# Performance work log

Hardware: AMD Instinct MI355X
Metric: run time of the kernel (lower is better)

## Reference

```python
import jax, jax.numpy as jnp
import numpy as np

NU, NS, NT = 200000, 100000, 100000
N = NS + NU + NT          # node order: [source items | users | target items]
D = 32                    # embedding_size
K = 3                     # graph_layer_K
DK = D * (K + 1)          # 128, concat of all propagation layers
META = 64                 # meta_dim
B = 2048                  # batch
L = 50                    # padded history length
NNZ = 2000000             # nnz of normalized adjacency


def setup_inputs() -> dict:
    key = jax.random.key(0)
    ks = jax.random.split(key, 32)
    f = lambda i, shape, s=0.05: jax.random.normal(ks[i], shape, jnp.float32) * s
    z = lambda shape: jnp.zeros(shape, jnp.float32)
    return dict(
        u=jax.random.randint(ks[0], (B,), 0, NU, jnp.int32),
        si=jax.random.randint(ks[1], (B,), 0, NS, jnp.int32),
        ti=jax.random.randint(ks[2], (B,), 0, NT, jnp.int32),
        src_seq=jax.random.randint(ks[3], (NU, L), 0, NS, jnp.int32),
        tgt_seq=jax.random.randint(ks[4], (NU, L), 0, NT, jnp.int32),
        adj_rows=jax.random.randint(ks[5], (NNZ,), 0, N, jnp.int32),
        adj_cols=jax.random.randint(ks[6], (NNZ,), 0, N, jnp.int32),
        adj_vals=jax.random.uniform(ks[7], (NNZ,), jnp.float32) * 0.1,
        user_emb=f(8, (NU, D), 0.1),
        item_s_emb=f(9, (NS, D), 0.1),
        item_t_emb=f(10, (NT, D), 0.1),
        attn_s_w1=f(11, (D, D)), attn_s_b1=z((D,)), attn_s_w2=f(12, (D, 1)),
        attn_t_w1=f(13, (D, D)), attn_t_b1=z((D,)), attn_t_w2=f(14, (D, 1)),
        dec_ss_w1=f(15, (D, META)), dec_ss_b1=z((META,)),
        dec_ss_w2=f(16, (META, DK * DK), 0.02), dec_ss_b2=z((DK * DK,)),
        dec_tt_w1=f(17, (D, META)), dec_tt_b1=z((META,)),
        dec_tt_w2=f(18, (META, DK * DK), 0.02), dec_tt_b2=z((DK * DK,)),
        mlp_s_w1=f(19, (2 * DK, 128)), mlp_s_b1=z((128,)),
        mlp_s_w2=f(20, (128, 64)), mlp_s_b2=z((64,)),
        dense_s_w=f(21, (64, 1)), dense_s_b=z((1,)),
        mlp_t_w1=f(22, (2 * DK, 128)), mlp_t_b1=z((128,)),
        mlp_t_w2=f(23, (128, 64)), mlp_t_b2=z((64,)),
        dense_t_w=f(24, (64, 1)), dense_t_b=z((1,)),
    )


def _attn_pool(seq_ids, item_emb, w1, b1, w2):
    # masked attention pooling over padded history; pad id is 0
    e = item_emb[seq_ids]                          # [B,L,D]
    h = jax.nn.relu(e @ w1 + b1)                   # attention_layer_K = 1
    logits = h @ w2                                # [B,L,1], no bias on final layer
    mask = (seq_ids == 0)[..., None].astype(e.dtype)
    att = jax.nn.softmax(logits - mask * 1e8, axis=1)
    return jnp.sum(att * e, axis=1)                # [B,D]


def _meta_decode(his, w1, b1, w2, b2, u_e):
    # meta-generated per-sample DKxDK transform applied to the user embedding
    W = (jax.nn.relu(his @ w1 + b1) @ w2 + b2).reshape(-1, DK, DK)
    return jnp.einsum('bd,bde->be', u_e, W)


def _ncf(x, w1, b1, w2, b2, dw, db):
    h = jax.nn.relu(x @ w1 + b1)
    h = jax.nn.relu(h @ w2 + b2)
    return jax.nn.sigmoid(h @ dw + db)[:, 0]


def reference(u, si, ti, src_seq, tgt_seq, adj_rows, adj_cols, adj_vals,
              user_emb, item_s_emb, item_t_emb,
              attn_s_w1, attn_s_b1, attn_s_w2, attn_t_w1, attn_t_b1, attn_t_w2,
              dec_ss_w1, dec_ss_b1, dec_ss_w2, dec_ss_b2,
              dec_tt_w1, dec_tt_b1, dec_tt_w2, dec_tt_b2,
              mlp_s_w1, mlp_s_b1, mlp_s_w2, mlp_s_b2, dense_s_w, dense_s_b,
              mlp_t_w1, mlp_t_b1, mlp_t_w2, mlp_t_b2, dense_t_w, dense_t_b):
    his_s = _attn_pool(src_seq[u], item_s_emb, attn_s_w1, attn_s_b1, attn_s_w2)
    his_t = _attn_pool(tgt_seq[u], item_t_emb, attn_t_w1, attn_t_b1, attn_t_w2)

    # 'raw' graph encoder: K hops of sparse A @ E over [item_s | user | item_t]
    emb = jnp.concatenate([item_s_emb, user_emb, item_t_emb], axis=0)  # [N,D]
    all_emb = [emb]
    for _ in range(K):
        emb = jax.ops.segment_sum(adj_vals[:, None] * emb[adj_cols], adj_rows,
                                  num_segments=N)
        all_emb.append(emb)
    all_e = jnp.concatenate(all_emb, axis=1)       # [N, DK]

    si_e = all_e[si]                               # source items: rows [0, NS)
    u_e = all_e[NS + u]                            # users: rows [NS, NS+NU)
    ti_e = all_e[NS + NU + ti]                     # target items

    u_ss = _meta_decode(his_s, dec_ss_w1, dec_ss_b1, dec_ss_w2, dec_ss_b2, u_e)
    u_tt = _meta_decode(his_t, dec_tt_w1, dec_tt_b1, dec_tt_w2, dec_tt_b2, u_e)

    pred_s = _ncf(jnp.concatenate([u_ss, si_e], -1),
                  mlp_s_w1, mlp_s_b1, mlp_s_w2, mlp_s_b2, dense_s_w, dense_s_b)
    pred_t = _ncf(jnp.concatenate([u_tt, ti_e], -1),
                  mlp_t_w1, mlp_t_b1, mlp_t_w2, mlp_t_b2, dense_t_w, dense_t_b)
    return jnp.stack([pred_s, pred_t])             # [2, B]
```

## Files before the change

kernel.cpp:

```cpp
#include <hip/hip_runtime.h>
#include <hip/hip_bf16.h>

#define NU_ 200000
#define NS_ 100000
#define NT_ 100000
#define NN_ (NS_ + NU_ + NT_)
#define D_ 32
#define DK_ 128
#define META_ 64
#define B_ 2048
#define L_ 50
#define NNZ_ 2000000
#define GK_ 8192

#define RPB_ 391
#define NB_ 1024
#define STAGE_CAP_ 4096
#define CAPA_ 1280
#define CAPB_ 512

#define SB_EMB_   6250
#define IN4_SLOT3_ 100096
#define IN4_MARKS_ 50048
#define IN4_E3C_   49152
#define IN4_TOT_  (IN4_SLOT3_ + IN4_MARKS_ + IN4_E3C_)
#define SB_INIT_  ((IN4_TOT_ + 2048 + 255) / 256)
#define SB_TOT_   (SB_EMB_ + SB_INIT_)

#define PB_GATHER_ 192
#define PB_HRELU_  (PB_GATHER_ + 1024)
#define PB_TOT_    (PB_HRELU_ + 1024)

#define NCF_TILE_ 16

typedef __attribute__((ext_vector_type(8))) short bf16x8;
typedef __attribute__((ext_vector_type(4))) float f32x4;

__device__ inline unsigned bfpack(float a, float b) {
    unsigned r;
    asm("v_cvt_pk_bf16_f32 %0, %1, %2" : "=v"(r) : "v"(a), "v"(b));
    return r;
}
__device__ inline float bf2f(short s) {
    return __uint_as_float(((unsigned)(unsigned short)s) << 16);
}

__global__ __launch_bounds__(256) void setup_kernel(
    const float* __restrict__ item_s, const float* __restrict__ user_e,
    const float* __restrict__ item_t, unsigned short* __restrict__ tab,
    int* __restrict__ slot3, int* __restrict__ marks ,
    float* __restrict__ E3c, int* __restrict__ bcurA, int* __restrict__ bcurB)
{
    int bid = blockIdx.x, t = threadIdx.x;
    if (bid < SB_EMB_) {
        int tid = bid * 256 + t;
        int row = tid >> 2, seg = tid & 3;
        const float* src;
        if (row < NS_)            src = item_s + (size_t)row * 32;
        else if (row < NS_ + NU_) src = user_e + (size_t)(row - NS_) * 32;
        else                      src = item_t + (size_t)(row - NS_ - NU_) * 32;
        const float4* sp = (const float4*)(src + seg * 8);
        float4 a = sp[0], b = sp[1];
        uint4 r;
        r.x = bfpack(a.x, a.y); r.y = bfpack(a.z, a.w);
        r.z = bfpack(b.x, b.y); r.w = bfpack(b.z, b.w);
        *(uint4*)(tab + (size_t)row * 32 + seg * 8) = r;
    } else {
        int idx = (bid - SB_EMB_) * 256 + t;
        if (idx < IN4_SLOT3_) {
            ((int4*)slot3)[idx] = make_int4(-1, -1, -1, -1);
        } else if (idx < IN4_SLOT3_ + IN4_MARKS_) {
            ((int4*)marks)[idx - IN4_SLOT3_] = make_int4(0, 0, 0, 0);
        } else if (idx < IN4_TOT_) {
            ((int4*)E3c)[idx - IN4_SLOT3_ - IN4_MARKS_] = make_int4(0, 0, 0, 0);
        } else {
            int c = idx - IN4_TOT_;
            if (c < NB_)            bcurA[c] = c * CAPA_;
            else if (c < 2 * NB_)   bcurB[c - NB_] = (c - NB_) * CAPB_;
        }
    }
}

__global__ __launch_bounds__(256) void mark_seeds(
    const int* __restrict__ u, const int* __restrict__ si, const int* __restrict__ ti,
    int* __restrict__ slot3, unsigned char* __restrict__ mark1,
    unsigned char* __restrict__ mark2)
{
    int n = blockIdx.x * 256 + threadIdx.x;
    if (n >= 3 * B_) return;
    int which = n >> 11, b = n & (B_ - 1);
    int row = (which == 0) ? si[b] : (which == 1) ? NS_ + u[b] : NS_ + NU_ + ti[b];
    slot3[row] = n;
    mark1[row] = 1;
    mark2[row] = 1;
}

__global__ __launch_bounds__(256) void mark_pass(
    const int* __restrict__ rows, const int* __restrict__ cols,
    const int* __restrict__ slot3, const unsigned char* __restrict__ msrc,
    unsigned char* __restrict__ mdst, int use_slot)
{
    int j = blockIdx.x * 256 + threadIdx.x;
    if (j >= NNZ_) return;
    int r = rows[j];
    bool cond = use_slot ? (slot3[r] >= 0) : (msrc[r] != 0);
    if (cond) mdst[cols[j]] = 1;
}

__global__ __launch_bounds__(512) void partition_edges(
    const int* __restrict__ rows, const int* __restrict__ cols,
    const float* __restrict__ vals,
    const unsigned char* __restrict__ mark1, const unsigned char* __restrict__ mark2,
    int* __restrict__ bcurA, int* __restrict__ bcurB,
    int2* __restrict__ partA, int2* __restrict__ partB)
{
    __shared__ int hist[NB_], sstart[NB_], sbase[NB_], scur[NB_];
    __shared__ int2 stage[STAGE_CAP_];
    __shared__ unsigned short stageb[STAGE_CAP_];
    __shared__ int stotal;

    int t = threadIdx.x;
    for (int i = t; i < NB_; i += 512) hist[i] = 0;
    __syncthreads();

    int base = blockIdx.x * 8192;
    int mybkt[16]; int2 mye[16]; unsigned myB = 0;
    #pragma unroll
    for (int i = 0; i < 16; i++) {
        int j = base + i * 512 + t;
        mybkt[i] = -1;
        if (j < NNZ_) {
            int r = rows[j];
            if (mark1[r]) {
                int bb = r / RPB_;
                int lr = r - bb * RPB_;
                mye[i] = make_int2((lr << 19) | cols[j], __float_as_int(vals[j]));
                mybkt[i] = bb;
                if (mark2[r]) myB |= (1u << i);
                atomicAdd(&hist[bb], 1);
            }
        }
    }
    __syncthreads();
    for (int i = t; i < NB_; i += 512) sstart[i] = hist[i];
    __syncthreads();
    for (int off = 1; off < NB_; off <<= 1) {
        int x0 = (t >= off) ? sstart[t - off] : 0;
        int x1 = (t + 512 >= off) ? sstart[t + 512 - off] : 0;
        __syncthreads();
        sstart[t] += x0; sstart[t + 512] += x1;
        __syncthreads();
    }
    if (t == 0) stotal = sstart[NB_ - 1];
    __syncthreads();
    int tot = stotal;
    for (int i = t; i < NB_; i += 512) {
        int cnt = hist[i];
        sstart[i] -= cnt;
        sbase[i] = cnt ? atomicAdd(&bcurA[i], cnt) : 0;
        scur[i] = 0;
    }
    __syncthreads();

    if (tot <= STAGE_CAP_) {
        #pragma unroll
        for (int i = 0; i < 16; i++) {
            int bb = mybkt[i];
            if (bb >= 0) {
                int p = atomicAdd(&scur[bb], 1);
                int s = sstart[bb] + p;
                stage[s] = mye[i];
                stageb[s] = (unsigned short)bb;
            }
        }
        __syncthreads();
        for (int i = t; i < tot; i += 512) {
            int bb = stageb[i];
            int pos = sbase[bb] + (i - sstart[bb]);
            if (pos < (bb + 1) * CAPA_) partA[pos] = stage[i];
        }
    } else {
        #pragma unroll
        for (int i = 0; i < 16; i++) {
            int bb = mybkt[i];
            if (bb >= 0) {
                int p = atomicAdd(&scur[bb], 1);
                int pos = sbase[bb] + p;
                if (pos < (bb + 1) * CAPA_) partA[pos] = mye[i];
            }
        }
    }
    __syncthreads();
    for (int i = t; i < NB_; i += 512) hist[i] = 0;
    __syncthreads();
    #pragma unroll
    for (int i = 0; i < 16; i++)
        if (myB & (1u << i)) atomicAdd(&hist[mybkt[i]], 1);
    __syncthreads();
    for (int i = t; i < NB_; i += 512) {
        sbase[i] = hist[i] ? atomicAdd(&bcurB[i], hist[i]) : 0;
        scur[i] = 0;
    }
    __syncthreads();
    #pragma unroll
    for (int i = 0; i < 16; i++) {
        if (myB & (1u << i)) {
            int bb = mybkt[i];
            int p = atomicAdd(&scur[bb], 1);
            int pos = sbase[bb] + p;
            if (pos < (bb + 1) * CAPB_) partB[pos] = mye[i];
        }
    }
}

__global__ __launch_bounds__(512) void hop_csr(
    const int* __restrict__ bcur, const int2* __restrict__ part, int cap,
    const unsigned short* __restrict__ tab,
    const unsigned char* __restrict__ markw,
    const int* __restrict__ fgate,
    float* __restrict__ yf, unsigned short* __restrict__ ybf)
{
    __shared__ int2 sorted[CAPA_];
    __shared__ int cnt[RPB_];
    __shared__ int scanb[512];

    int t = threadIdx.x;
    int bkt = blockIdx.x;
    int e0 = bkt * cap;
    int n = bcur[bkt] - e0;
    if (n > cap) n = cap;

    for (int i = t; i < RPB_; i += 512) cnt[i] = 0;
    __syncthreads();
    for (int i = t; i < n; i += 512) {
        int lr = (part[e0 + i].x >> 19) & 0x3FF;
        atomicAdd(&cnt[lr], 1);
    }
    __syncthreads();
    scanb[t] = (t < RPB_) ? cnt[t] : 0;
    __syncthreads();
    for (int off = 1; off < 512; off <<= 1) {
        int x = (t >= off) ? scanb[t - off] : 0;
        __syncthreads();
        scanb[t] += x;
        __syncthreads();
    }
    if (t < RPB_) cnt[t] = scanb[t] - cnt[t];
    __syncthreads();
    for (int i = t; i < n; i += 512) {
        int2 e = part[e0 + i];
        int lr = (e.x >> 19) & 0x3FF;
        int p2 = atomicAdd(&cnt[lr], 1);
        sorted[p2] = e;
    }
    __syncthreads();
    int chunk = t & 3;
    int row0 = bkt * RPB_;
    for (int r = t >> 2; r < RPB_; r += 128) {
        int grow = row0 + r;
        if (grow >= NN_ || !markw[grow]) continue;
        int eb = (r == 0) ? 0 : scanb[r - 1];
        int ee = scanb[r];
        float racc[8] = {0.f, 0.f, 0.f, 0.f, 0.f, 0.f, 0.f, 0.f};
        for (int e = eb; e < ee; e++) {
            int2 ed = sorted[e];
            int col = ed.x & 0x7FFFF;
            float vv = __int_as_float(ed.y);
            bf16x8 x = *(const bf16x8*)(tab + (size_t)col * 32 + chunk * 8);
            #pragma unroll
            for (int k = 0; k < 8; k++) racc[k] += vv * bf2f(x[k]);
        }
        float4 o0 = {racc[0], racc[1], racc[2], racc[3]};
        float4 o1 = {racc[4], racc[5], racc[6], racc[7]};
        if (!fgate || fgate[grow] >= 0) {
            float4* yp = (float4*)(yf + (size_t)grow * 32 + chunk * 8);
            yp[0] = o0; yp[1] = o1;
        }
        if (ybf) {
            uint4 pk;
            pk.x = bfpack(o0.x, o0.y); pk.y = bfpack(o0.z, o0.w);
            pk.z = bfpack(o1.x, o1.y); pk.w = bfpack(o1.z, o1.w);
            *(uint4*)(ybf + (size_t)grow * 32 + chunk * 8) = pk;
        }
    }
}

__global__ __launch_bounds__(256) void hop3_part(
    const int* __restrict__ bcurB, const int2* __restrict__ partB,
    const int* __restrict__ slot3,
    const float* __restrict__ E2, float* __restrict__ E3c)
{
    int t = threadIdx.x;
    int bkt = blockIdx.x;
    int e0 = bkt * CAPB_;
    int e1 = bcurB[bkt];
    int emax = e0 + CAPB_;
    if (e1 > emax) e1 = emax;
    int c = t & 7;
    for (int i = e0 + (t >> 3); i < e1; i += 32) {
        int2 e = partB[i];
        int lr = (e.x >> 19) & 0x3FF;
        int s = slot3[bkt * RPB_ + lr];
        if (s < 0) continue;
        int col = e.x & 0x7FFFF;
        float v = __int_as_float(e.y);
        float4 xv = ((const float4*)E2)[(size_t)col * 8 + c];
        float* p = E3c + (size_t)s * 32 + c * 4;
        unsafeAtomicAdd(p + 0, v * xv.x);
        unsafeAtomicAdd(p + 1, v * xv.y);
        unsafeAtomicAdd(p + 2, v * xv.z);
        unsafeAtomicAdd(p + 3, v * xv.w);
    }
}

__global__ __launch_bounds__(64) void attn_pool(
    const int* __restrict__ u,
    const int* __restrict__ seq_s, const int* __restrict__ seq_t,
    const float* __restrict__ emb_s, const float* __restrict__ emb_t,
    const float* __restrict__ w1_s, const float* __restrict__ b1_s,
    const float* __restrict__ w2_s,
    const float* __restrict__ w1_t, const float* __restrict__ b1_t,
    const float* __restrict__ w2_t,
    float* __restrict__ out_s, float* __restrict__ out_t)
{
    int b = blockIdx.x, dom = blockIdx.y;
    const int* seq = dom ? seq_t : seq_s;
    const float* emb = dom ? emb_t : emb_s;
    const float* w1 = dom ? w1_t : w1_s;
    const float* b1 = dom ? b1_t : b1_s;
    const float* w2 = dom ? w2_t : w2_s;
    float* out = dom ? out_t : out_s;

    int l = threadIdx.x;
    __shared__ float w1s[32 * 32];
    __shared__ float b1s[32];
    __shared__ float w2s[32];
    __shared__ float es[L_ * 32];
    __shared__ float att[64];

    for (int i = l; i < 1024; i += 64) w1s[i] = w1[i];
    if (l < 32) { b1s[l] = b1[l]; w2s[l] = w2[l]; }
    __syncthreads();

    int uid = u[b];
    float logit = -1e30f;
    if (l < L_) {
        int id = seq[uid * L_ + l];
        const float4* ep = (const float4*)(emb + (size_t)id * 32);
        float e[32];
        #pragma unroll
        for (int q = 0; q < 8; q++) {
            float4 v = ep[q];
            e[4*q+0] = v.x; e[4*q+1] = v.y; e[4*q+2] = v.z; e[4*q+3] = v.w;
        }
        float acc = 0.f;
        #pragma unroll
        for (int i = 0; i < 32; i++) {
            float h = b1s[i];
            #pragma unroll
            for (int jj = 0; jj < 32; jj++) h += e[jj] * w1s[jj * 32 + i];
            h = fmaxf(h, 0.f);
            acc += h * w2s[i];
        }
        logit = acc - (id == 0 ? 1e8f : 0.f);
        #pragma unroll
        for (int jj = 0; jj < 32; jj++) es[l * 32 + jj] = e[jj];
    }
    float m = logit;
    for (int off = 32; off > 0; off >>= 1) m = fmaxf(m, __shfl_down(m, off, 64));
    m = __shfl(m, 0, 64);
    float ex = (l < L_) ? expf(logit - m) : 0.f;
    float s = ex;
    for (int off = 32; off > 0; off >>= 1) s += __shfl_down(s, off, 64);
    s = __shfl(s, 0, 64);
    att[l] = ex / s;
    __syncthreads();

    if (l < 32) {
        float o = 0.f;
        for (int q = 0; q < L_; q++) o += att[q] * es[q * 32 + l];
        out[b * 32 + l] = o;
    }
}

__global__ __launch_bounds__(256) void prep_kernel(
    const float* __restrict__ E1, const float* __restrict__ E2,
    const float* __restrict__ E3c, const int* __restrict__ slot3,
    const int* __restrict__ u, const int* __restrict__ si, const int* __restrict__ ti,
    const float* __restrict__ user_emb, const float* __restrict__ item_s,
    const float* __restrict__ item_t,
    float* __restrict__ u_e, float* __restrict__ si_e, float* __restrict__ ti_e,
    const float* __restrict__ his_s, const float* __restrict__ his_t,
    const float* __restrict__ dw1_s, const float* __restrict__ db1_s,
    const float* __restrict__ dw1_t, const float* __restrict__ db1_t,
    float* __restrict__ h_s, float* __restrict__ h_t,
    const float* __restrict__ w2_s, const float* __restrict__ w2_t,
    unsigned short* __restrict__ o_s, unsigned short* __restrict__ o_t)
{
    int bid = blockIdx.x, t = threadIdx.x;
    if (bid < PB_GATHER_) {
        int tid = bid * 256 + t;
        if (tid >= 3 * B_ * 8) return;
        int n = tid >> 3, c = tid & 7;
        int which = n >> 11, b = n & (B_ - 1);
        int row;
        const float4* base0;
        float* outp;
        if (which == 0)      { int id = si[b]; row = id;             base0 = (const float4*)item_s + (size_t)id * 8; outp = si_e; }
        else if (which == 1) { int id = u[b];  row = NS_ + id;       base0 = (const float4*)user_emb + (size_t)id * 8; outp = u_e; }
        else                 { int id = ti[b]; row = NS_ + NU_ + id; base0 = (const float4*)item_t + (size_t)id * 8; outp = ti_e; }
        float4 k0 = base0[c];
        float4 k1 = ((const float4*)E1)[(size_t)row * 8 + c];
        float4 k2 = ((const float4*)E2)[(size_t)row * 8 + c];
        float4 k3 = ((const float4*)E3c)[(size_t)slot3[row] * 8 + c];
        float4* orow = (float4*)(outp + (size_t)b * 128);
        orow[0 * 8 + c] = k0;
        orow[1 * 8 + c] = k1;
        orow[2 * 8 + c] = k2;
        orow[3 * 8 + c] = k3;
    } else if (bid < PB_HRELU_) {
        int b2 = bid - PB_GATHER_;
        int dom = b2 >> 9, sub = b2 & 511;
        const float* his = dom ? his_t : his_s;
        const float* w1  = dom ? dw1_t : dw1_s;
        const float* b1  = dom ? db1_t : db1_s;
        float* h         = dom ? h_t   : h_s;
        int b = sub * 4 + (t >> 6);
        int m = t & 63;
        float acc = b1[m];
        #pragma unroll
        for (int j = 0; j < 32; j++) acc += his[b * 32 + j] * w1[j * 64 + m];
        h[b * 64 + m] = fmaxf(acc, 0.f);
    } else {
        int b3 = bid - PB_HRELU_;
        int dom = b3 >> 9, sub = b3 & 511;
        const float* w2 = dom ? w2_t : w2_s;
        unsigned short* o = dom ? o_t : o_s;
        int tid = sub * 256 + t;
        int nn = tid & 127, k8 = tid >> 7;
        float v[8];
        #pragma unroll
        for (int i = 0; i < 8; i++) v[i] = w2[(size_t)(k8 * 8 + i) * 128 + nn];
        uint4 r;
        r.x = bfpack(v[0], v[1]); r.y = bfpack(v[2], v[3]);
        r.z = bfpack(v[4], v[5]); r.w = bfpack(v[6], v[7]);
        *(uint4*)(o + (size_t)nn * GK_ + k8 * 8) = r;
    }
}

__global__ __launch_bounds__(256) void meta_gemm(
    const float* __restrict__ h_s, const float* __restrict__ h_t,
    const float* __restrict__ ue,
    const unsigned short* __restrict__ w2t_s, const unsigned short* __restrict__ w2t_t,
    float* __restrict__ P)
{
    __shared__ unsigned short As[64 * 72];
    __shared__ unsigned short Bs[128 * 72];

    int mt = blockIdx.x & 31, dom = blockIdx.x >> 5;
    int ks = blockIdx.y;
    const float* h = dom ? h_t : h_s;
    const unsigned short* w2t = dom ? w2t_t : w2t_s;

    int t = threadIdx.x;
    int ar = t >> 2, aseg = t & 3;
    int bn = t >> 1, bhalf = t & 1;
    int w = t >> 6, lane = t & 63;
    int quad = lane >> 4, l16 = lane & 15;
    int wm = (w & 1) * 32, wn = (w >> 1) * 64;

    f32x4 acc[8];
    #pragma unroll
    for (int i = 0; i < 8; i++) { acc[i][0]=0.f; acc[i][1]=0.f; acc[i][2]=0.f; acc[i][3]=0.f; }

    for (int ch = 0; ch < 16; ch++) {
        int kb = ks * 1024 + ch * 64;
        __syncthreads();
        {
            int gm = mt * 64 + ar;
            int m_idx = kb >> 7;
            int d0 = (kb & 127) + aseg * 16;
            float hv = h[gm * 64 + m_idx];
            const float4* up = (const float4*)(ue + (size_t)gm * 128 + d0);
            float4 x0 = up[0], x1 = up[1], x2 = up[2], x3 = up[3];
            uint4 A0, A1;
            A0.x = bfpack(hv*x0.x, hv*x0.y); A0.y = bfpack(hv*x0.z, hv*x0.w);
            A0.z = bfpack(hv*x1.x, hv*x1.y); A0.w = bfpack(hv*x1.z, hv*x1.w);
            A1.x = bfpack(hv*x2.x, hv*x2.y); A1.y = bfpack(hv*x2.z, hv*x2.w);
            A1.z = bfpack(hv*x3.x, hv*x3.y); A1.w = bfpack(hv*x3.z, hv*x3.w);
            uint4* sa = (uint4*)(As + ar * 72 + aseg * 16);
            sa[0] = A0; sa[1] = A1;
        }
        {
            const uint4* gb = (const uint4*)(w2t + (size_t)bn * GK_ + kb + bhalf * 32);
            uint4* sb = (uint4*)(Bs + bn * 72 + bhalf * 32);
            sb[0] = gb[0]; sb[1] = gb[1]; sb[2] = gb[2]; sb[3] = gb[3];
        }
        __syncthreads();
        #pragma unroll
        for (int kk = 0; kk < 2; kk++) {
            int ko = kk * 32 + quad * 8;
            bf16x8 a0 = *(const bf16x8*)(As + (wm + l16) * 72 + ko);
            bf16x8 a1 = *(const bf16x8*)(As + (wm + 16 + l16) * 72 + ko);
            #pragma unroll
            for (int nt = 0; nt < 4; nt++) {
                bf16x8 bfr = *(const bf16x8*)(Bs + (wn + nt * 16 + l16) * 72 + ko);
                acc[nt]     = __builtin_amdgcn_mfma_f32_16x16x32_bf16(a0, bfr, acc[nt],     0, 0, 0);
                acc[4 + nt] = __builtin_amdgcn_mfma_f32_16x16x32_bf16(a1, bfr, acc[4 + nt], 0, 0, 0);
            }
        }
    }
    float* op = P + ((size_t)dom * 8 + ks) * B_ * 128;
    #pragma unroll
    for (int ma = 0; ma < 2; ma++)
        #pragma unroll
        for (int nt = 0; nt < 4; nt++) {
            int row = mt * 64 + wm + ma * 16 + quad * 4;
            int col = wn + nt * 16 + l16;
            f32x4 v = acc[ma * 4 + nt];
            op[(size_t)(row + 0) * 128 + col] = v[0];
            op[(size_t)(row + 1) * 128 + col] = v[1];
            op[(size_t)(row + 2) * 128 + col] = v[2];
            op[(size_t)(row + 3) * 128 + col] = v[3];
        }
}

__global__ __launch_bounds__(512) void ncf_kernel(
    const float* __restrict__ P, const float* __restrict__ u_e,
    const float* __restrict__ b2_s, const float* __restrict__ b2_t,
    const float* __restrict__ si_e, const float* __restrict__ ti_e,
    const float* __restrict__ w1_s, const float* __restrict__ b1_s,
    const float* __restrict__ w2_s, const float* __restrict__ bb2_s,
    const float* __restrict__ dw_s, const float* __restrict__ db_s,
    const float* __restrict__ w1_t, const float* __restrict__ b1_t,
    const float* __restrict__ w2_t, const float* __restrict__ bb2_t,
    const float* __restrict__ dw_t, const float* __restrict__ db_t,
    float* __restrict__ out)
{
    int tile = blockIdx.x, dom = blockIdx.y, t = threadIdx.x;
    int b0 = tile * NCF_TILE_;
    const float* Pd     = P + (size_t)dom * 8 * B_ * 128;
    const float* b2meta = dom ? b2_t : b2_s;
    const float* pair_e = dom ? ti_e : si_e;
    const float* w1 = dom ? w1_t : w1_s;
    const float* b1 = dom ? b1_t : b1_s;
    const float* w2 = dom ? w2_t : w2_s;
    const float* bb2 = dom ? bb2_t : bb2_s;
    const float* dw = dom ? dw_t : dw_s;
    const float* db = dom ? db_t : db_s;

    __shared__ float ues[NCF_TILE_ * 128];
    __shared__ float xs[NCF_TILE_ * 256];
    __shared__ float h1s[NCF_TILE_ * 128];
    __shared__ float h2s[NCF_TILE_ * 64];

    {
        float4 v = ((const float4*)(u_e + (size_t)b0 * 128))[t];
        ((float4*)ues)[t] = v;
        float4 pv = ((const float4*)(pair_e + (size_t)b0 * 128))[t];
        int s = t >> 5, c4 = t & 31;
        ((float4*)(xs + s * 256 + 128))[c4] = pv;
    }
    __syncthreads();

    int j = t & 127, g = t >> 7;
    {
        float acc[4];
        #pragma unroll
        for (int ss = 0; ss < 4; ss++) {
            int b = b0 + g * 4 + ss;
            float a = 0.f;
            #pragma unroll
            for (int ks = 0; ks < 8; ks++)
                a += Pd[(size_t)ks * B_ * 128 + (size_t)b * 128 + j];
            acc[ss] = a;
        }
        for (int dc = 0; dc < 32; dc++) {
            float wa = b2meta[(dc * 4 + 0) * 128 + j];
            float wb = b2meta[(dc * 4 + 1) * 128 + j];
            float wc = b2meta[(dc * 4 + 2) * 128 + j];
            float wd = b2meta[(dc * 4 + 3) * 128 + j];
            #pragma unroll
            for (int ss = 0; ss < 4; ss++) {
                float4 uv = ((const float4*)(ues + (g * 4 + ss) * 128))[dc];
                acc[ss] += uv.x * wa + uv.y * wb + uv.z * wc + uv.w * wd;
            }
        }
        #pragma unroll
        for (int ss = 0; ss < 4; ss++) xs[(g * 4 + ss) * 256 + j] = acc[ss];
    }
    __syncthreads();

    {
        float b1v = b1[j];
        float acc[4] = {b1v, b1v, b1v, b1v};
        for (int kc = 0; kc < 64; kc++) {
            float wa = w1[(kc * 4 + 0) * 128 + j];
            float wb = w1[(kc * 4 + 1) * 128 + j];
            float wc = w1[(kc * 4 + 2) * 128 + j];
            float wd = w1[(kc * 4 + 3) * 128 + j];
            #pragma unroll
            for (int ss = 0; ss < 4; ss++) {
                float4 xv = ((const float4*)(xs + (g * 4 + ss) * 256))[kc];
                acc[ss] += xv.x * wa + xv.y * wb + xv.z * wc + xv.w * wd;
            }
        }
        #pragma unroll
        for (int ss = 0; ss < 4; ss++)
            h1s[(g * 4 + ss) * 128 + j] = fmaxf(acc[ss], 0.f);
    }
    __syncthreads();

    {
        int m = t & 63, g2 = t >> 6;
        float bv = bb2[m];
        float acc[2] = {bv, bv};
        for (int kc = 0; kc < 32; kc++) {
            float wa = w2[(kc * 4 + 0) * 64 + m];
            float wb = w2[(kc * 4 + 1) * 64 + m];
            float wc = w2[(kc * 4 + 2) * 64 + m];
            float wd = w2[(kc * 4 + 3) * 64 + m];
            #pragma unroll
            for (int ss = 0; ss < 2; ss++) {
                float4 hv = ((const float4*)(h1s + (g2 * 2 + ss) * 128))[kc];
                acc[ss] += hv.x * wa + hv.y * wb + hv.z * wc + hv.w * wd;
            }
        }
        #pragma unroll
        for (int ss = 0; ss < 2; ss++)
            h2s[(g2 * 2 + ss) * 64 + m] = fmaxf(acc[ss], 0.f);
    }
    __syncthreads();

    {
        int s = t >> 5, l = t & 31;
        float sum = h2s[s * 64 + l] * dw[l] + h2s[s * 64 + 32 + l] * dw[32 + l];
        #pragma unroll
        for (int off = 16; off > 0; off >>= 1) sum += __shfl_down(sum, off, 32);
        if (l == 0) {
            float z = sum + db[0];
            out[(size_t)dom * B_ + b0 + s] = 1.f / (1.f + expf(-z));
        }
    }
}

extern "C" void kernel_launch(void* const* d_in, const int* in_sizes, int n_in,
                              void* d_out, int out_size, void* d_ws, size_t ws_size,
                              hipStream_t stream)
{
    const int*   u          = (const int*)  d_in[0];
    const int*   si         = (const int*)  d_in[1];
    const int*   ti         = (const int*)  d_in[2];
    const int*   src_seq    = (const int*)  d_in[3];
    const int*   tgt_seq    = (const int*)  d_in[4];
    const int*   adj_rows   = (const int*)  d_in[5];
    const int*   adj_cols   = (const int*)  d_in[6];
    const float* adj_vals   = (const float*)d_in[7];
    const float* user_emb   = (const float*)d_in[8];
    const float* item_s_emb = (const float*)d_in[9];
    const float* item_t_emb = (const float*)d_in[10];
    const float* attn_s_w1  = (const float*)d_in[11];
    const float* attn_s_b1  = (const float*)d_in[12];
    const float* attn_s_w2  = (const float*)d_in[13];
    const float* attn_t_w1  = (const float*)d_in[14];
    const float* attn_t_b1  = (const float*)d_in[15];
    const float* attn_t_w2  = (const float*)d_in[16];
    const float* dec_ss_w1  = (const float*)d_in[17];
    const float* dec_ss_b1  = (const float*)d_in[18];
    const float* dec_ss_w2  = (const float*)d_in[19];
    const float* dec_ss_b2  = (const float*)d_in[20];
    const float* dec_tt_w1  = (const float*)d_in[21];
    const float* dec_tt_b1  = (const float*)d_in[22];
    const float* dec_tt_w2  = (const float*)d_in[23];
    const float* dec_tt_b2  = (const float*)d_in[24];
    const float* mlp_s_w1   = (const float*)d_in[25];
    const float* mlp_s_b1   = (const float*)d_in[26];
    const float* mlp_s_w2   = (const float*)d_in[27];
    const float* mlp_s_b2   = (const float*)d_in[28];
    const float* dense_s_w  = (const float*)d_in[29];
    const float* dense_s_b  = (const float*)d_in[30];
    const float* mlp_t_w1   = (const float*)d_in[31];
    const float* mlp_t_b1   = (const float*)d_in[32];
    const float* mlp_t_w2   = (const float*)d_in[33];
    const float* mlp_t_b2   = (const float*)d_in[34];
    const float* dense_t_w  = (const float*)d_in[35];
    const float* dense_t_b  = (const float*)d_in[36];

    char* p = (char*)d_ws;
    float* E1    = (float*)p;              p += (size_t)NN_ * 32 * 4;
    float* E2    = (float*)p;              p += (size_t)NN_ * 32 * 4;
    unsigned short* Ebf  = (unsigned short*)p; p += (size_t)NN_ * 32 * 2;
    unsigned short* E1bf = (unsigned short*)p; p += (size_t)NN_ * 32 * 2;
    int2*  partA = (int2*)p;               p += (size_t)NB_ * CAPA_ * 8;
    int2*  partB = (int2*)p;               p += (size_t)NB_ * CAPB_ * 8;
    int*   slot3 = (int*)p;                p += (size_t)400384 * 4;
    int*   marks = (int*)p;
    unsigned char* mark1 = (unsigned char*)p; p += 400384;
    unsigned char* mark2 = (unsigned char*)p; p += 400384;
    float* E3c   = (float*)p;              p += (size_t)3 * B_ * 32 * 4;
    int*   bcurA = (int*)p;                p += NB_ * 4;
    int*   bcurB = (int*)p;                p += NB_ * 4;
    float* his_s = (float*)p;              p += (size_t)B_ * 32 * 4;
    float* his_t = (float*)p;              p += (size_t)B_ * 32 * 4;
    float* u_e   = (float*)p;              p += (size_t)B_ * 128 * 4;
    float* si_e  = (float*)p;              p += (size_t)B_ * 128 * 4;
    float* ti_e  = (float*)p;              p += (size_t)B_ * 128 * 4;
    float* h_s   = (float*)p;              p += (size_t)B_ * 64 * 4;
    float* h_t   = (float*)p;              p += (size_t)B_ * 64 * 4;
    float* P     = (float*)p;              p += (size_t)2 * 8 * B_ * 128 * 4;
    unsigned short* w2t_s = (unsigned short*)p; p += (size_t)128 * GK_ * 2;
    unsigned short* w2t_t = (unsigned short*)p; p += (size_t)128 * GK_ * 2;

    int nnzBlocks = (NNZ_ + 255) / 256;

    setup_kernel<<<SB_TOT_, 256, 0, stream>>>(item_s_emb, user_emb, item_t_emb,
                                              Ebf, slot3, marks, E3c, bcurA, bcurB);
    mark_seeds<<<24, 256, 0, stream>>>(u, si, ti, slot3, mark1, mark2);
    mark_pass<<<nnzBlocks, 256, 0, stream>>>(adj_rows, adj_cols, slot3, mark2, mark2, 1);
    mark_pass<<<nnzBlocks, 256, 0, stream>>>(adj_rows, adj_cols, slot3, mark2, mark1, 0);
    partition_edges<<<245, 512, 0, stream>>>(adj_rows, adj_cols, adj_vals,
                                             mark1, mark2, bcurA, bcurB, partA, partB);
    hop_csr<<<NB_, 512, 0, stream>>>(bcurA, partA, CAPA_, Ebf,  mark1, slot3, E1, E1bf);
    hop_csr<<<NB_, 512, 0, stream>>>(bcurB, partB, CAPB_, E1bf, mark2, nullptr, E2, nullptr);
    hop3_part<<<NB_, 256, 0, stream>>>(bcurB, partB, slot3, E2, E3c);
    attn_pool<<<dim3(B_, 2), 64, 0, stream>>>(u, src_seq, tgt_seq,
                                              item_s_emb, item_t_emb,
                                              attn_s_w1, attn_s_b1, attn_s_w2,
                                              attn_t_w1, attn_t_b1, attn_t_w2,
                                              his_s, his_t);
    prep_kernel<<<PB_TOT_, 256, 0, stream>>>(E1, E2, E3c, slot3, u, si, ti,
                                             user_emb, item_s_emb, item_t_emb,
                                             u_e, si_e, ti_e,
                                             his_s, his_t,
                                             dec_ss_w1, dec_ss_b1,
                                             dec_tt_w1, dec_tt_b1, h_s, h_t,
                                             dec_ss_w2, dec_tt_w2, w2t_s, w2t_t);
    meta_gemm<<<dim3(64, 8), 256, 0, stream>>>(h_s, h_t, u_e, w2t_s, w2t_t, P);
    ncf_kernel<<<dim3(B_ / NCF_TILE_, 2), 512, 0, stream>>>(P, u_e, dec_ss_b2, dec_tt_b2,
                                                si_e, ti_e,
                                                mlp_s_w1, mlp_s_b1, mlp_s_w2, mlp_s_b2,
                                                dense_s_w, dense_s_b,
                                                mlp_t_w1, mlp_t_b1, mlp_t_w2, mlp_t_b2,
                                                dense_t_w, dense_t_b,
                                                (float*)d_out);
}
```

Measured before the change: 421.1 us.

## Fold attention pooling and W2 transpose into setup kernel; register-cache edges in hop_csr

The attention-pooling kernel is merged into setup_kernel as extra blocks, each handling four batch rows with one wave apiece, and the decoder W2 bf16 transpose moves from prep_kernel into setup_kernel as well. This drops one launch and lets independent work share the first kernel's grid. hop_csr now loads each thread's up to three edges into registers once and reuses them for both the counting and scatter passes, avoiding a second global read of the partition. setup_kernel's shared memory grows, since every block allocates the attention buffers, which may lower occupancy for the large embedding-conversion part of its grid.

```diff
diff --git a/kernel.cpp b/kernel.cpp
--- a/kernel.cpp
+++ b/kernel.cpp
@@ -26,10 +26,12 @@
 #define IN4_TOT_  (IN4_SLOT3_ + IN4_MARKS_ + IN4_E3C_)
 #define SB_INIT_  ((IN4_TOT_ + 2048 + 255) / 256)
 #define SB_TOT_   (SB_EMB_ + SB_INIT_)
+#define SB_ATT0_  SB_TOT_
+#define SB_W2C0_  (SB_TOT_ + 1024)
+#define SB_GRID_  (SB_W2C0_ + 1024)
 
 #define PB_GATHER_ 192
-#define PB_HRELU_  (PB_GATHER_ + 1024)
-#define PB_TOT_    (PB_HRELU_ + 1024)
+#define PB_TOT_    (PB_GATHER_ + 1024)
 
 #define NCF_TILE_ 16
 
@@ -49,8 +51,23 @@
     const float* __restrict__ item_s, const float* __restrict__ user_e,
     const float* __restrict__ item_t, unsigned short* __restrict__ tab,
     int* __restrict__ slot3, int* __restrict__ marks ,
-    float* __restrict__ E3c, int* __restrict__ bcurA, int* __restrict__ bcurB)
-{
+    float* __restrict__ E3c, int* __restrict__ bcurA, int* __restrict__ bcurB,
+    const int* __restrict__ u,
+    const int* __restrict__ seq_s, const int* __restrict__ seq_t,
+    const float* __restrict__ aw1_s, const float* __restrict__ ab1_s,
+    const float* __restrict__ aw2_s,
+    const float* __restrict__ aw1_t, const float* __restrict__ ab1_t,
+    const float* __restrict__ aw2_t,
+    float* __restrict__ his_s, float* __restrict__ his_t,
+    const float* __restrict__ dw2_s, const float* __restrict__ dw2_t,
+    unsigned short* __restrict__ o_s, unsigned short* __restrict__ o_t)
+{
+    __shared__ float w1s[1024];
+    __shared__ float b1s[32];
+    __shared__ float w2s[32];
+    __shared__ float es[4][L_ * 32];
+    __shared__ float att[4][64];
+
     int bid = blockIdx.x, t = threadIdx.x;
     if (bid < SB_EMB_) {
         int tid = bid * 256 + t;
@@ -65,7 +82,7 @@
         r.x = bfpack(a.x, a.y); r.y = bfpack(a.z, a.w);
         r.z = bfpack(b.x, b.y); r.w = bfpack(b.z, b.w);
         *(uint4*)(tab + (size_t)row * 32 + seg * 8) = r;
-    } else {
+    } else if (bid < SB_TOT_) {
         int idx = (bid - SB_EMB_) * 256 + t;
         if (idx < IN4_SLOT3_) {
             ((int4*)slot3)[idx] = make_int4(-1, -1, -1, -1);
@@ -78,6 +95,75 @@
             if (c < NB_)            bcurA[c] = c * CAPA_;
             else if (c < 2 * NB_)   bcurB[c - NB_] = (c - NB_) * CAPB_;
         }
+    } else if (bid < SB_W2C0_) {
+        int aid = bid - SB_ATT0_;
+        int dom = aid >> 9;
+        const int* seq = dom ? seq_t : seq_s;
+        const float* emb = dom ? item_t : item_s;
+        const float* w1 = dom ? aw1_t : aw1_s;
+        const float* b1 = dom ? ab1_t : ab1_s;
+        const float* w2 = dom ? aw2_t : aw2_s;
+        float* out = dom ? his_t : his_s;
+
+        for (int i = t; i < 1024; i += 256) w1s[i] = w1[i];
+        if (t < 32) { b1s[t] = b1[t]; w2s[t] = w2[t]; }
+        __syncthreads();
+
+        int w = t >> 6, l = t & 63;
+        int b = (aid & 511) * 4 + w;
+        int uid = u[b];
+        float logit = -1e30f;
+        if (l < L_) {
+            int id = seq[uid * L_ + l];
+            const float4* ep = (const float4*)(emb + (size_t)id * 32);
+            float e[32];
+            #pragma unroll
+            for (int q = 0; q < 8; q++) {
+                float4 v = ep[q];
+                e[4*q+0] = v.x; e[4*q+1] = v.y; e[4*q+2] = v.z; e[4*q+3] = v.w;
+            }
+            float acc = 0.f;
+            #pragma unroll
+            for (int i = 0; i < 32; i++) {
+                float h = b1s[i];
+                #pragma unroll
+                for (int jj = 0; jj < 32; jj++) h += e[jj] * w1s[jj * 32 + i];
+                h = fmaxf(h, 0.f);
+                acc += h * w2s[i];
+            }
+            logit = acc - (id == 0 ? 1e8f : 0.f);
+            #pragma unroll
+            for (int jj = 0; jj < 32; jj++) es[w][l * 32 + jj] = e[jj];
+        }
+        float m = logit;
+        for (int off = 32; off > 0; off >>= 1) m = fmaxf(m, __shfl_down(m, off, 64));
+        m = __shfl(m, 0, 64);
+        float ex = (l < L_) ? expf(logit - m) : 0.f;
+        float s = ex;
+        for (int off = 32; off > 0; off >>= 1) s += __shfl_down(s, off, 64);
+        s = __shfl(s, 0, 64);
+        att[w][l] = ex / s;
+        __syncthreads();
+
+        if (l < 32) {
+            float o = 0.f;
+            for (int q = 0; q < L_; q++) o += att[w][q] * es[w][q * 32 + l];
+            out[b * 32 + l] = o;
+        }
+    } else {
+        int b3 = bid - SB_W2C0_;
+        int dom = b3 >> 9, sub = b3 & 511;
+        const float* w2 = dom ? dw2_t : dw2_s;
+        unsigned short* o = dom ? o_t : o_s;
+        int tid = sub * 256 + t;
+        int nn = tid & 127, k8 = tid >> 7;
+        float v[8];
+        #pragma unroll
+        for (int i = 0; i < 8; i++) v[i] = w2[(size_t)(k8 * 8 + i) * 128 + nn];
+        uint4 r;
+        r.x = bfpack(v[0], v[1]); r.y = bfpack(v[2], v[3]);
+        r.z = bfpack(v[4], v[5]); r.w = bfpack(v[6], v[7]);
+        *(uint4*)(o + (size_t)nn * GK_ + k8 * 8) = r;
     }
 }
 
@@ -230,12 +316,21 @@
     int n = bcur[bkt] - e0;
     if (n > cap) n = cap;
 
+    int2 mye[3]; int myl[3];
+    #pragma unroll
+    for (int i = 0; i < 3; i++) {
+        int j = i * 512 + t;
+        myl[i] = -1;
+        if (j < n) {
+            mye[i] = part[e0 + j];
+            myl[i] = (mye[i].x >> 19) & 0x3FF;
+        }
+    }
     for (int i = t; i < RPB_; i += 512) cnt[i] = 0;
     __syncthreads();
-    for (int i = t; i < n; i += 512) {
-        int lr = (part[e0 + i].x >> 19) & 0x3FF;
-        atomicAdd(&cnt[lr], 1);
-    }
+    #pragma unroll
+    for (int i = 0; i < 3; i++)
+        if (myl[i] >= 0) atomicAdd(&cnt[myl[i]], 1);
     __syncthreads();
     scanb[t] = (t < RPB_) ? cnt[t] : 0;
     __syncthreads();
@@ -247,12 +342,12 @@
     }
     if (t < RPB_) cnt[t] = scanb[t] - cnt[t];
     __syncthreads();
-    for (int i = t; i < n; i += 512) {
-        int2 e = part[e0 + i];
-        int lr = (e.x >> 19) & 0x3FF;
-        int p2 = atomicAdd(&cnt[lr], 1);
-        sorted[p2] = e;
-    }
+    #pragma unroll
+    for (int i = 0; i < 3; i++)
+        if (myl[i] >= 0) {
+            int p2 = atomicAdd(&cnt[myl[i]], 1);
+            sorted[p2] = mye[i];
+        }
     __syncthreads();
     int chunk = t & 3;
     int row0 = bkt * RPB_;
@@ -313,76 +408,6 @@
     }
 }
 
-__global__ __launch_bounds__(64) void attn_pool(
-    const int* __restrict__ u,
-    const int* __restrict__ seq_s, const int* __restrict__ seq_t,
-    const float* __restrict__ emb_s, const float* __restrict__ emb_t,
-    const float* __restrict__ w1_s, const float* __restrict__ b1_s,
-    const float* __restrict__ w2_s,
-    const float* __restrict__ w1_t, const float* __restrict__ b1_t,
-    const float* __restrict__ w2_t,
-    float* __restrict__ out_s, float* __restrict__ out_t)
-{
-    int b = blockIdx.x, dom = blockIdx.y;
-    const int* seq = dom ? seq_t : seq_s;
-    const float* emb = dom ? emb_t : emb_s;
-    const float* w1 = dom ? w1_t : w1_s;
-    const float* b1 = dom ? b1_t : b1_s;
-    const float* w2 = dom ? w2_t : w2_s;
-    float* out = dom ? out_t : out_s;
-
-    int l = threadIdx.x;
-    __shared__ float w1s[32 * 32];
-    __shared__ float b1s[32];
-    __shared__ float w2s[32];
-    __shared__ float es[L_ * 32];
-    __shared__ float att[64];
-
-    for (int i = l; i < 1024; i += 64) w1s[i] = w1[i];
-    if (l < 32) { b1s[l] = b1[l]; w2s[l] = w2[l]; }
-    __syncthreads();
-
-    int uid = u[b];
-    float logit = -1e30f;
-    if (l < L_) {
-        int id = seq[uid * L_ + l];
-        const float4* ep = (const float4*)(emb + (size_t)id * 32);
-        float e[32];
-        #pragma unroll
-        for (int q = 0; q < 8; q++) {
-            float4 v = ep[q];
-            e[4*q+0] = v.x; e[4*q+1] = v.y; e[4*q+2] = v.z; e[4*q+3] = v.w;
-        }
-        float acc = 0.f;
-        #pragma unroll
-        for (int i = 0; i < 32; i++) {
-            float h = b1s[i];
-            #pragma unroll
-            for (int jj = 0; jj < 32; jj++) h += e[jj] * w1s[jj * 32 + i];
-            h = fmaxf(h, 0.f);
-            acc += h * w2s[i];
-        }
-        logit = acc - (id == 0 ? 1e8f : 0.f);
-        #pragma unroll
-        for (int jj = 0; jj < 32; jj++) es[l * 32 + jj] = e[jj];
-    }
-    float m = logit;
-    for (int off = 32; off > 0; off >>= 1) m = fmaxf(m, __shfl_down(m, off, 64));
-    m = __shfl(m, 0, 64);
-    float ex = (l < L_) ? expf(logit - m) : 0.f;
-    float s = ex;
-    for (int off = 32; off > 0; off >>= 1) s += __shfl_down(s, off, 64);
-    s = __shfl(s, 0, 64);
-    att[l] = ex / s;
-    __syncthreads();
-
-    if (l < 32) {
-        float o = 0.f;
-        for (int q = 0; q < L_; q++) o += att[q] * es[q * 32 + l];
-        out[b * 32 + l] = o;
-    }
-}
-
 __global__ __launch_bounds__(256) void prep_kernel(
     const float* __restrict__ E1, const float* __restrict__ E2,
     const float* __restrict__ E3c, const int* __restrict__ slot3,
@@ -393,9 +418,7 @@
     const float* __restrict__ his_s, const float* __restrict__ his_t,
     const float* __restrict__ dw1_s, const float* __restrict__ db1_s,
     const float* __restrict__ dw1_t, const float* __restrict__ db1_t,
-    float* __restrict__ h_s, float* __restrict__ h_t,
-    const float* __restrict__ w2_s, const float* __restrict__ w2_t,
-    unsigned short* __restrict__ o_s, unsigned short* __restrict__ o_t)
+    float* __restrict__ h_s, float* __restrict__ h_t)
 {
     int bid = blockIdx.x, t = threadIdx.x;
     if (bid < PB_GATHER_) {
@@ -418,7 +441,7 @@
         orow[1 * 8 + c] = k1;
         orow[2 * 8 + c] = k2;
         orow[3 * 8 + c] = k3;
-    } else if (bid < PB_HRELU_) {
+    } else {
         int b2 = bid - PB_GATHER_;
         int dom = b2 >> 9, sub = b2 & 511;
         const float* his = dom ? his_t : his_s;
@@ -431,20 +454,6 @@
         #pragma unroll
         for (int j = 0; j < 32; j++) acc += his[b * 32 + j] * w1[j * 64 + m];
         h[b * 64 + m] = fmaxf(acc, 0.f);
-    } else {
-        int b3 = bid - PB_HRELU_;
-        int dom = b3 >> 9, sub = b3 & 511;
-        const float* w2 = dom ? w2_t : w2_s;
-        unsigned short* o = dom ? o_t : o_s;
-        int tid = sub * 256 + t;
-        int nn = tid & 127, k8 = tid >> 7;
-        float v[8];
-        #pragma unroll
-        for (int i = 0; i < 8; i++) v[i] = w2[(size_t)(k8 * 8 + i) * 128 + nn];
-        uint4 r;
-        r.x = bfpack(v[0], v[1]); r.y = bfpack(v[2], v[3]);
-        r.z = bfpack(v[4], v[5]); r.w = bfpack(v[6], v[7]);
-        *(uint4*)(o + (size_t)nn * GK_ + k8 * 8) = r;
     }
 }
 
@@ -713,8 +722,13 @@
 
     int nnzBlocks = (NNZ_ + 255) / 256;
 
-    setup_kernel<<<SB_TOT_, 256, 0, stream>>>(item_s_emb, user_emb, item_t_emb,
-                                              Ebf, slot3, marks, E3c, bcurA, bcurB);
+    setup_kernel<<<SB_GRID_, 256, 0, stream>>>(item_s_emb, user_emb, item_t_emb,
+                                               Ebf, slot3, marks, E3c, bcurA, bcurB,
+                                               u, src_seq, tgt_seq,
+                                               attn_s_w1, attn_s_b1, attn_s_w2,
+                                               attn_t_w1, attn_t_b1, attn_t_w2,
+                                               his_s, his_t,
+                                               dec_ss_w2, dec_tt_w2, w2t_s, w2t_t);
     mark_seeds<<<24, 256, 0, stream>>>(u, si, ti, slot3, mark1, mark2);
     mark_pass<<<nnzBlocks, 256, 0, stream>>>(adj_rows, adj_cols, slot3, mark2, mark2, 1);
     mark_pass<<<nnzBlocks, 256, 0, stream>>>(adj_rows, adj_cols, slot3, mark2, mark1, 0);
@@ -723,18 +737,12 @@
     hop_csr<<<NB_, 512, 0, stream>>>(bcurA, partA, CAPA_, Ebf,  mark1, slot3, E1, E1bf);
     hop_csr<<<NB_, 512, 0, stream>>>(bcurB, partB, CAPB_, E1bf, mark2, nullptr, E2, nullptr);
     hop3_part<<<NB_, 256, 0, stream>>>(bcurB, partB, slot3, E2, E3c);
-    attn_pool<<<dim3(B_, 2), 64, 0, stream>>>(u, src_seq, tgt_seq,
-                                              item_s_emb, item_t_emb,
-                                              attn_s_w1, attn_s_b1, attn_s_w2,
-                                              attn_t_w1, attn_t_b1, attn_t_w2,
-                                              his_s, his_t);
     prep_kernel<<<PB_TOT_, 256, 0, stream>>>(E1, E2, E3c, slot3, u, si, ti,
                                              user_emb, item_s_emb, item_t_emb,
                                              u_e, si_e, ti_e,
                                              his_s, his_t,
                                              dec_ss_w1, dec_ss_b1,
-                                             dec_tt_w1, dec_tt_b1, h_s, h_t,
-                                             dec_ss_w2, dec_tt_w2, w2t_s, w2t_t);
+                                             dec_tt_w1, dec_tt_b1, h_s, h_t);
     meta_gemm<<<dim3(64, 8), 256, 0, stream>>>(h_s, h_t, u_e, w2t_s, w2t_t, P);
     ncf_kernel<<<dim3(B_ / NCF_TILE_, 2), 512, 0, stream>>>(P, u_e, dec_ss_b2, dec_tt_b2,
                                                 si_e, ti_e,
```

New measurement: 417.6 us. About the same (-0.8%).
